# Kernel optimization log

Hardware: AMD Instinct MI355X
Metric: run time of the kernel (lower is better)

The kernel has to match this reference:

```python
import jax, jax.numpy as jnp
import numpy as np

B, N, D, H, CH = 16, 2048, 2, 128, 32
NEG = -1e9


def setup_inputs() -> dict:
    key = jax.random.key(0)
    ks = jax.random.split(key, 24)
    u = lambda k, shape, fan_in: jax.random.uniform(k, shape, jnp.float32,
                                                    -1.0 / np.sqrt(fan_in), 1.0 / np.sqrt(fan_in))
    inp = {
        "features": jax.random.normal(ks[0], (B, N, D), jnp.float32),
        "adj": jax.random.randint(ks[1], (B, N, N), 0, 2, jnp.int32),
        "candidates": jax.random.randint(ks[2], (B, N), 0, 2, jnp.int32).at[:, 0].set(1),
        "action": jnp.zeros((B,), jnp.int32),
        # GCN encoder (3 layers)
        "W1": u(ks[3], (D, H), D), "b1": jnp.zeros((H,), jnp.float32),
        "W2": u(ks[4], (H, H), H), "b2": jnp.zeros((H,), jnp.float32),
        "W3": u(ks[5], (H, H), H), "b3": jnp.zeros((H,), jnp.float32),
        # learned machine state
        "machine_state": jax.random.uniform(ks[6], (H,), jnp.float32, -1.0, 1.0),
        # actor MLP: Linear(3H,H) -> ReLU -> Linear(H,H) -> ReLU -> Linear(H,1)
        "A1": u(ks[7], (3 * H, H), 3 * H), "ab1": u(ks[8], (H,), 3 * H),
        "A2": u(ks[9], (H, H), H), "ab2": u(ks[10], (H,), H),
        "A3": u(ks[11], (H, 1), H), "ab3": u(ks[12], (1,), H),
        # critic MLP: Linear(H,CH) -> ReLU -> Linear(CH,1)
        "C1": u(ks[13], (H, CH), H), "cb1": u(ks[14], (CH,), H),
        "C2": u(ks[15], (CH, 1), CH), "cb2": u(ks[16], (1,), CH),
    }
    return inp


def _gcn_propagation_matrix(adj):
    # Faithful to PyG GCNConv(add_self_loops=True) fed edges from dense_to_sparse
    # with edge attrs discarded (all weights 1).
    A = (adj != 0).astype(jnp.float32)                      # (B,N,N), A[b,j,i]: edge j->i
    A = jnp.maximum(A, jnp.eye(N, dtype=jnp.float32))       # add_remaining_self_loops
    deg = A.sum(axis=1)                                     # (B,N) incoming degree per target i
    dis = jax.lax.rsqrt(deg)                                # deg >= 1 due to self loops
    # S[b,j,i] = dis[j] * A[j,i] * dis[i]
    return dis[:, :, None] * A * dis[:, None, :]


def reference(features, adj, candidates, action,
              W1, b1, W2, b2, W3, b3, machine_state,
              A1, ab1, A2, ab2, A3, ab3, C1, cb1, C2, cb2):
    S = _gcn_propagation_matrix(adj)
    h = features
    for W, b in ((W1, b1), (W2, b2), (W3, b3)):
        # out[b,i,:] = sum_j S[b,j,i] * (h W)[b,j,:]
        h = jax.nn.relu(jnp.einsum('bji,bjd->bid', S, h @ W) + b)
    pool = h.mean(axis=1)                                   # (B,H) global mean pool

    concat = jnp.concatenate(
        [h,
         jnp.broadcast_to(pool[:, None, :], h.shape),
         jnp.broadcast_to(machine_state[None, None, :], h.shape)], axis=-1)  # (B,N,3H)
    a = jax.nn.relu(concat @ A1 + ab1)
    a = jax.nn.relu(a @ A2 + ab2)
    scores = ((a @ A3 + ab3)[..., 0]) * 10.0                # (B,N)

    probs_sm = jax.nn.softmax(scores, axis=1)               # softmax over jobs
    logits = jnp.where(candidates != 0, probs_sm, NEG)      # masked_fill(~candidates, -inf)
    logp = jax.nn.log_softmax(logits, axis=1)               # Categorical(logits=...)
    log_prob = jnp.take_along_axis(logp, action[:, None].astype(jnp.int32), axis=1)[:, 0]
    p = jnp.exp(logp)
    entropy = -(p * logp).sum(axis=1)

    value = jax.nn.relu(pool @ C1 + cb1) @ C2 + cb2         # (B,1)
    return action, log_prob, entropy, value
```

## Files before the change

### kernel.cpp

```cpp
#include <hip/hip_runtime.h>
#include <hip/hip_bf16.h>
#include <stdint.h>

#define B_  16
#define N_  2048
#define D_  2
#define H_  128
#define CH_ 32
#define NEG_ (-1e9f)

typedef __attribute__((ext_vector_type(8))) short bf16x8;
typedef __attribute__((ext_vector_type(4))) float f32x4;
typedef unsigned short u16;

__device__ inline u16 f2bf(float f){
    union { __hip_bfloat16 h; u16 u; } cv;
    cv.h = __float2bfloat16(f);
    return cv.u;
}
__device__ inline float bf2f(u16 v){ return __uint_as_float(((unsigned)v) << 16); }

__device__ inline void gld16(const u16* g, u16* l){
    __builtin_amdgcn_global_load_lds(
        (const __attribute__((address_space(1))) unsigned int*)(const void*)g,
        (__attribute__((address_space(3))) unsigned int*)(void*)l, 16, 0, 0);
}

__global__ __launch_bounds__(256) void k_prep(const int* __restrict__ adj,
                                              u16* __restrict__ ATbf,
                                              float* __restrict__ degF){
    int i0 = blockIdx.x * 64, j0 = blockIdx.y * 64, b = blockIdx.z;
    __shared__ u16 tile[64 * 72];
    __shared__ float degP[256];
    int t = threadIdx.x;
    const int* ap = adj + (size_t)b * N_ * N_;
    #pragma unroll
    for (int it = 0; it < 4; ++it){
        int jj = it * 16 + (t >> 4);
        int gi0 = (t & 15) * 4;
        int4 a4 = *(const int4*)&ap[(size_t)(j0 + jj) * N_ + i0 + gi0];
        int gj = j0 + jj;
        tile[(gi0 + 0) * 72 + jj] = (a4.x != 0 || gj == i0 + gi0 + 0) ? (u16)0x3F80 : (u16)0;
        tile[(gi0 + 1) * 72 + jj] = (a4.y != 0 || gj == i0 + gi0 + 1) ? (u16)0x3F80 : (u16)0;
        tile[(gi0 + 2) * 72 + jj] = (a4.z != 0 || gj == i0 + gi0 + 2) ? (u16)0x3F80 : (u16)0;
        tile[(gi0 + 3) * 72 + jj] = (a4.w != 0 || gj == i0 + gi0 + 3) ? (u16)0x3F80 : (u16)0;
    }
    __syncthreads();
    {
        int ii = t & 63, q = t >> 6;
        float s = 0.f;
        #pragma unroll
        for (int k = 0; k < 16; ++k) s += (tile[ii * 72 + q * 16 + k] ? 1.f : 0.f);
        degP[t] = s;
    }
    __syncthreads();
    if (t < 64){
        float s = degP[t] + degP[t + 64] + degP[t + 128] + degP[t + 192];
        atomicAdd(&degF[b * N_ + i0 + t], s);
    }
    u16* op = ATbf + (size_t)b * N_ * N_;
    #pragma unroll
    for (int it = 0; it < 2; ++it){
        int idx = it * 256 + t;
        int io = idx >> 3, jo = (idx & 7) * 8;
        *(uint4*)&op[(size_t)(i0 + io) * N_ + j0 + jo] = *(const uint4*)&tile[io * 72 + jo];
    }
}

__global__ __launch_bounds__(256) void k_misc(const float* __restrict__ degF,
                                              float* __restrict__ dis,
                                              const float* __restrict__ W2, u16* __restrict__ WT2,
                                              const float* __restrict__ W3, u16* __restrict__ WT3,
                                              const float* __restrict__ A1, u16* __restrict__ A1aT,
                                              const float* __restrict__ A2, u16* __restrict__ A2T){
    int bx = blockIdx.x;
    if (bx < 128){
        int i = bx * 256 + threadIdx.x;
        dis[i] = rsqrtf(degF[i]);
        return;
    }
    int q = (bx - 128) >> 6;
    const float* s; u16* d;
    switch (q){
        case 0: s = W2; d = WT2; break;
        case 1: s = W3; d = WT3; break;
        case 2: s = A1; d = A1aT; break;
        default: s = A2; d = A2T; break;
    }
    int idx = ((bx - 128) & 63) * 256 + threadIdx.x;
    int hp = idx >> 7, k = idx & 127;
    d[hp * 128 + k] = f2bf(s[k * 128 + hp]);
}

__global__ __launch_bounds__(256) void k_y1(const float* __restrict__ feat,
                                            const float* __restrict__ W1,
                                            const float* __restrict__ dis,
                                            u16* __restrict__ YT){
    int j = blockIdx.x * 256 + threadIdx.x;
    int h = blockIdx.y, b = blockIdx.z;
    float f0 = feat[((size_t)b * N_ + j) * D_ + 0];
    float f1 = feat[((size_t)b * N_ + j) * D_ + 1];
    float v = dis[b * N_ + j] * (f0 * W1[h] + f1 * W1[H_ + h]);
    YT[(size_t)b * H_ * N_ + (size_t)h * N_ + j] = f2bf(v);
}

template<int MODE>
__global__ __launch_bounds__(512) void k_layer(const u16* __restrict__ ATbf,
                                               const u16* __restrict__ Yin,
                                               const float* __restrict__ dis,
                                               const float* __restrict__ bias,
                                               const u16* __restrict__ WT,
                                               u16* __restrict__ Yout,
                                               u16* __restrict__ h3,
                                               float* __restrict__ poolF){
    int bid = blockIdx.x;
    int b = bid & 15, i0 = (bid >> 4) * 128;
    const u16* Ab = ATbf + (size_t)b * N_ * N_ + (size_t)i0 * N_;
    const u16* Bb = Yin  + (size_t)b * H_ * N_;
    __shared__ __align__(16) u16 ABs[16384];
    __shared__ __align__(16) u16 Hs[128 * 136];
    u16* As = ABs;
    u16* Bs = ABs + 8192;
    int t = threadIdx.x, w = t >> 6, lane = t & 63, quad = lane >> 4, l16 = lane & 15;
    int srow = lane >> 3, scol = (lane & 7) * 8;
    f32x4 acc[8];
    #pragma unroll
    for (int nt = 0; nt < 8; ++nt) acc[nt] = (f32x4){0.f, 0.f, 0.f, 0.f};

    for (int k0 = 0; k0 < N_; k0 += 64){
        #pragma unroll
        for (int it = 0; it < 4; ++it){
            int chunk = w * 4 + it;
            if (chunk < 16)
                gld16(Ab + (size_t)(chunk * 8 + srow) * N_ + k0 + scol, As + chunk * 512);
            else
                gld16(Bb + (size_t)((chunk - 16) * 8 + srow) * N_ + k0 + scol, Bs + (chunk - 16) * 512);
        }
        __syncthreads();
        #pragma unroll
        for (int kc = 0; kc < 2; ++kc){
            bf16x8 af = *(const bf16x8*)&As[(w * 16 + l16) * 64 + kc * 32 + quad * 8];
            #pragma unroll
            for (int nt = 0; nt < 8; ++nt){
                bf16x8 bv = *(const bf16x8*)&Bs[(nt * 16 + l16) * 64 + kc * 32 + quad * 8];
                acc[nt] = __builtin_amdgcn_mfma_f32_16x16x32_bf16(af, bv, acc[nt], 0, 0, 0);
            }
        }
        __syncthreads();
    }

    if (MODE == 0){
        #pragma unroll
        for (int it = 0; it < 4; ++it){
            int chunk = w * 4 + it;
            gld16(WT + (size_t)(chunk * 4 + (lane >> 4)) * 128 + (lane & 15) * 8,
                  ABs + chunk * 512);
        }
    }
    #pragma unroll
    for (int r = 0; r < 4; ++r){
        int m = w * 16 + quad * 4 + r;
        float dsc = dis[b * N_ + i0 + m];
        #pragma unroll
        for (int nt = 0; nt < 8; ++nt){
            int n = nt * 16 + l16;
            float v = dsc * acc[nt][r] + bias[n];
            Hs[m * 136 + n] = f2bf(v > 0.f ? v : 0.f);
        }
    }
    __syncthreads();

    if (MODE == 0){
        f32x4 a2[8];
        #pragma unroll
        for (int nt = 0; nt < 8; ++nt) a2[nt] = (f32x4){0.f, 0.f, 0.f, 0.f};
        #pragma unroll
        for (int kc = 0; kc < 4; ++kc){
            bf16x8 af = *(const bf16x8*)&Hs[(w * 16 + l16) * 136 + kc * 32 + quad * 8];
            #pragma unroll
            for (int nt = 0; nt < 8; ++nt){
                bf16x8 bv = *(const bf16x8*)&ABs[(nt * 16 + l16) * 128 + kc * 32 + quad * 8];
                a2[nt] = __builtin_amdgcn_mfma_f32_16x16x32_bf16(af, bv, a2[nt], 0, 0, 0);
            }
        }
        __syncthreads();
        #pragma unroll
        for (int r = 0; r < 4; ++r){
            int m = w * 16 + quad * 4 + r;
            float dsc = dis[b * N_ + i0 + m];
            #pragma unroll
            for (int nt = 0; nt < 8; ++nt)
                Hs[m * 136 + nt * 16 + l16] = f2bf(dsc * a2[nt][r]);
        }
        __syncthreads();
        size_t obase = (size_t)b * H_ * N_ + i0;
        int j = t & 127, hq = t >> 7;
        #pragma unroll 8
        for (int rep = 0; rep < 32; ++rep){
            int hrow = hq + rep * 4;
            Yout[obase + (size_t)hrow * N_ + j] = Hs[j * 136 + hrow];
        }
    } else {
        #pragma unroll
        for (int rep = 0; rep < 4; ++rep){
            int idx = rep * 512 + t;
            int row = idx >> 3, col = (idx & 7) * 8;
            *(uint4*)&h3[((size_t)b * N_ + i0 + row) * H_ + col] = *(const uint4*)&Hs[row * 136 + col];
        }
        __shared__ float pred[512];
        int n = t & 127, rq = t >> 7;
        float ps = 0.f;
        #pragma unroll 8
        for (int r = 0; r < 32; ++r) ps += bf2f(Hs[(rq * 32 + r) * 136 + n]);
        pred[t] = ps;
        __syncthreads();
        if (t < 128)
            atomicAdd(&poolF[b * H_ + t],
                      (pred[t] + pred[t + 128] + pred[t + 256] + pred[t + 384]) * (1.f / N_));
    }
}

__global__ __launch_bounds__(256) void k_cv(const float* __restrict__ poolF,
                                            const float* __restrict__ ms,
                                            const float* __restrict__ A1,
                                            const float* __restrict__ ab1,
                                            const float* __restrict__ C1,
                                            const float* __restrict__ cb1,
                                            const float* __restrict__ C2,
                                            const float* __restrict__ cb2,
                                            float* __restrict__ cvec,
                                            float* __restrict__ out){
    int b = blockIdx.x, t = threadIdx.x;
    __shared__ float pl[128], msl[128], v1[32];
    if (t < 128){ pl[t] = poolF[b * H_ + t]; msl[t] = ms[t]; }
    __syncthreads();
    if (t < 128){
        float c = ab1[t];
        for (int k = 0; k < 128; ++k)
            c += pl[k] * A1[(128 + k) * H_ + t] + msl[k] * A1[(256 + k) * H_ + t];
        cvec[b * H_ + t] = c;
    } else if (t < 160){
        int cc = t - 128;
        float v = cb1[cc];
        for (int k = 0; k < 128; ++k) v += pl[k] * C1[k * CH_ + cc];
        v1[cc] = v > 0.f ? v : 0.f;
    }
    __syncthreads();
    if (t == 0){
        float v = cb2[0];
        for (int c = 0; c < CH_; ++c) v += v1[c] * C2[c];
        out[48 + b] = v;
    }
}

__global__ __launch_bounds__(256) void k_actor(const u16* __restrict__ h3,
                                               const u16* __restrict__ A1aT,
                                               const u16* __restrict__ A2T,
                                               const float* __restrict__ cvec,
                                               const float* __restrict__ ab2,
                                               const float* __restrict__ A3,
                                               const float* __restrict__ ab3,
                                               float* __restrict__ scores){
    int b = blockIdx.x, i0 = blockIdx.y * 128;
    const u16* Ab = h3 + ((size_t)b * N_ + i0) * H_;
    __shared__ __align__(16) u16 As[128 * 72];
    __shared__ __align__(16) u16 Bs[128 * 72];
    __shared__ __align__(16) u16 M1[128 * 136];
    __shared__ float sLDS[128];
    int t = threadIdx.x, w = t >> 6, lane = t & 63, quad = lane >> 4, l16 = lane & 15;
    int sr = t >> 3, sc = (t & 7) * 8;
    f32x4 acc[2][8];
    #pragma unroll
    for (int mt = 0; mt < 2; ++mt)
        #pragma unroll
        for (int nt = 0; nt < 8; ++nt) acc[mt][nt] = (f32x4){0.f, 0.f, 0.f, 0.f};
    for (int k0 = 0; k0 < H_; k0 += 64){
        #pragma unroll
        for (int it = 0; it < 4; ++it){
            int r = sr + it * 32;
            *(uint4*)&As[r * 72 + sc] = *(const uint4*)&Ab[(size_t)r * H_ + k0 + sc];
            *(uint4*)&Bs[r * 72 + sc] = *(const uint4*)&A1aT[(size_t)r * H_ + k0 + sc];
        }
        __syncthreads();
        #pragma unroll
        for (int kc = 0; kc < 2; ++kc){
            bf16x8 af[2];
            #pragma unroll
            for (int mt = 0; mt < 2; ++mt)
                af[mt] = *(const bf16x8*)&As[(w * 32 + mt * 16 + l16) * 72 + kc * 32 + quad * 8];
            #pragma unroll
            for (int nt = 0; nt < 8; ++nt){
                bf16x8 bfr = *(const bf16x8*)&Bs[(nt * 16 + l16) * 72 + kc * 32 + quad * 8];
                #pragma unroll
                for (int mt = 0; mt < 2; ++mt)
                    acc[mt][nt] = __builtin_amdgcn_mfma_f32_16x16x32_bf16(af[mt], bfr, acc[mt][nt], 0, 0, 0);
            }
        }
        __syncthreads();
    }
    const float* cv = cvec + b * H_;
    #pragma unroll
    for (int mt = 0; mt < 2; ++mt)
        #pragma unroll
        for (int r = 0; r < 4; ++r){
            int m = w * 32 + mt * 16 + quad * 4 + r;
            #pragma unroll
            for (int nt = 0; nt < 8; ++nt){
                int n = nt * 16 + l16;
                float v = acc[mt][nt][r] + cv[n];
                M1[m * 136 + n] = f2bf(v > 0.f ? v : 0.f);
                acc[mt][nt][r] = 0.f;
            }
        }
    if (t < 128) sLDS[t] = 0.f;
    for (int k0 = 0; k0 < H_; k0 += 64){
        #pragma unroll
        for (int it = 0; it < 4; ++it){
            int r = sr + it * 32;
            *(uint4*)&Bs[r * 72 + sc] = *(const uint4*)&A2T[(size_t)r * H_ + k0 + sc];
        }
        __syncthreads();
        #pragma unroll
        for (int kc = 0; kc < 2; ++kc){
            bf16x8 af[2];
            #pragma unroll
            for (int mt = 0; mt < 2; ++mt)
                af[mt] = *(const bf16x8*)&M1[(w * 32 + mt * 16 + l16) * 136 + k0 + kc * 32 + quad * 8];
            #pragma unroll
            for (int nt = 0; nt < 8; ++nt){
                bf16x8 bfr = *(const bf16x8*)&Bs[(nt * 16 + l16) * 72 + kc * 32 + quad * 8];
                #pragma unroll
                for (int mt = 0; mt < 2; ++mt)
                    acc[mt][nt] = __builtin_amdgcn_mfma_f32_16x16x32_bf16(af[mt], bfr, acc[mt][nt], 0, 0, 0);
            }
        }
        __syncthreads();
    }
    #pragma unroll
    for (int mt = 0; mt < 2; ++mt)
        #pragma unroll
        for (int r = 0; r < 4; ++r){
            int m = w * 32 + mt * 16 + quad * 4 + r;
            float part = 0.f;
            #pragma unroll
            for (int nt = 0; nt < 8; ++nt){
                int n = nt * 16 + l16;
                float v = acc[mt][nt][r] + ab2[n];
                v = v > 0.f ? v : 0.f;
                part += v * A3[n];
            }
            atomicAdd(&sLDS[m], part);
        }
    __syncthreads();
    if (t < 128) scores[(size_t)b * N_ + i0 + t] = (sLDS[t] + ab3[0]) * 10.f;
}

__device__ inline float wredS(float v){
    #pragma unroll
    for (int o = 32; o; o >>= 1) v += __shfl_xor(v, o, 64);
    return v;
}
__device__ inline float wredM(float v){
    #pragma unroll
    for (int o = 32; o; o >>= 1) v = fmaxf(v, __shfl_xor(v, o, 64));
    return v;
}

__global__ __launch_bounds__(256) void k_sm(const float* __restrict__ scores,
                                            const int* __restrict__ cand,
                                            const int* __restrict__ action,
                                            float* __restrict__ out){
    int b = blockIdx.x, t = threadIdx.x;
    __shared__ float sc[N_];
    __shared__ float red[4];
    __shared__ float lps;
    const float* sp = scores + (size_t)b * N_;
    const int*   cp = cand   + (size_t)b * N_;
    float mx = -1e30f;
    for (int i = t; i < N_; i += 256){ float v = sp[i]; sc[i] = v; mx = fmaxf(mx, v); }
    mx = wredM(mx);
    if ((t & 63) == 0) red[t >> 6] = mx;
    __syncthreads();
    mx = fmaxf(fmaxf(red[0], red[1]), fmaxf(red[2], red[3]));
    __syncthreads();
    float se = 0.f;
    for (int i = t; i < N_; i += 256) se += expf(sc[i] - mx);
    se = wredS(se);
    if ((t & 63) == 0) red[t >> 6] = se;
    __syncthreads();
    float s1 = red[0] + red[1] + red[2] + red[3];
    __syncthreads();
    float inv = 1.f / s1;
    float m2 = -1e30f;
    for (int i = t; i < N_; i += 256){
        float p = expf(sc[i] - mx) * inv;
        sc[i] = p;
        if (cp[i] != 0) m2 = fmaxf(m2, p);
    }
    m2 = wredM(m2);
    if ((t & 63) == 0) red[t >> 6] = m2;
    __syncthreads();
    m2 = fmaxf(fmaxf(red[0], red[1]), fmaxf(red[2], red[3]));
    __syncthreads();
    float s2 = 0.f;
    for (int i = t; i < N_; i += 256) if (cp[i] != 0) s2 += expf(sc[i] - m2);
    s2 = wredS(s2);
    if ((t & 63) == 0) red[t >> 6] = s2;
    __syncthreads();
    float lse = m2 + logf(red[0] + red[1] + red[2] + red[3]);
    __syncthreads();
    int a = action[b];
    float ent = 0.f;
    for (int i = t; i < N_; i += 256){
        float lp = (cp[i] != 0 ? sc[i] : NEG_) - lse;
        float pe = expf(lp);
        ent -= pe * lp;
        if (i == a) lps = lp;
    }
    ent = wredS(ent);
    if ((t & 63) == 0) red[t >> 6] = ent;
    __syncthreads();
    if (t == 0){
        out[b]      = (float)a;
        out[16 + b] = lps;
        out[32 + b] = red[0] + red[1] + red[2] + red[3];
    }
}

extern "C" void kernel_launch(void* const* d_in, const int* in_sizes, int n_in,
                              void* d_out, int out_size, void* d_ws, size_t ws_size,
                              hipStream_t stream) {
    const float* feat = (const float*)d_in[0];
    const int*   adj  = (const int*)d_in[1];
    const int*   cand = (const int*)d_in[2];
    const int*   act  = (const int*)d_in[3];
    const float* W1   = (const float*)d_in[4];
    const float* b1   = (const float*)d_in[5];
    const float* W2   = (const float*)d_in[6];
    const float* b2   = (const float*)d_in[7];
    const float* W3   = (const float*)d_in[8];
    const float* b3   = (const float*)d_in[9];
    const float* ms   = (const float*)d_in[10];
    const float* A1   = (const float*)d_in[11];
    const float* ab1  = (const float*)d_in[12];
    const float* A2   = (const float*)d_in[13];
    const float* ab2  = (const float*)d_in[14];
    const float* A3   = (const float*)d_in[15];
    const float* ab3  = (const float*)d_in[16];
    const float* C1   = (const float*)d_in[17];
    const float* cb1  = (const float*)d_in[18];
    const float* C2   = (const float*)d_in[19];
    const float* cb2  = (const float*)d_in[20];
    float* out = (float*)d_out;

    char* w8 = (char*)d_ws;
    size_t off = 0;
    auto alloc = [&](size_t bytes){ void* p = w8 + off; off += (bytes + 255) & ~(size_t)255; return p; };
    u16*   ATbf  = (u16*)  alloc((size_t)B_ * N_ * N_ * 2);
    u16*   YTa   = (u16*)  alloc((size_t)B_ * H_ * N_ * 2);
    u16*   YTb   = (u16*)  alloc((size_t)B_ * H_ * N_ * 2);
    u16*   hbuf  = (u16*)  alloc((size_t)B_ * N_ * H_ * 2);
    float* degF  = (float*)alloc((size_t)B_ * N_ * 4);
    float* poolF = (float*)alloc((size_t)B_ * H_ * 4);
    float* dis   = (float*)alloc((size_t)B_ * N_ * 4);
    float* cvec  = (float*)alloc((size_t)B_ * H_ * 4);
    float* scr   = (float*)alloc((size_t)B_ * N_ * 4);
    u16*   WT2   = (u16*)  alloc((size_t)H_ * H_ * 2);
    u16*   WT3   = (u16*)  alloc((size_t)H_ * H_ * 2);
    u16*   A1aT  = (u16*)  alloc((size_t)H_ * H_ * 2);
    u16*   A2T   = (u16*)  alloc((size_t)H_ * H_ * 2);

    hipMemsetAsync(degF, 0, (size_t)B_ * N_ * 4 + (size_t)B_ * H_ * 4, stream);

    k_prep<<<dim3(32, 32, 16), 256, 0, stream>>>(adj, ATbf, degF);
    k_misc<<<dim3(384), 256, 0, stream>>>(degF, dis, W2, WT2, W3, WT3, A1, A1aT, A2, A2T);
    k_y1  <<<dim3(8, 128, 16), 256, 0, stream>>>(feat, W1, dis, YTa);

    k_layer<0><<<dim3(256), 512, 0, stream>>>(ATbf, YTa, dis, b1, WT2, YTb, nullptr, nullptr);
    k_layer<0><<<dim3(256), 512, 0, stream>>>(ATbf, YTb, dis, b2, WT3, YTa, nullptr, nullptr);
    k_layer<1><<<dim3(256), 512, 0, stream>>>(ATbf, YTa, dis, b3, nullptr, nullptr, hbuf, poolF);

    k_cv  <<<dim3(16), 256, 0, stream>>>(poolF, ms, A1, ab1, C1, cb1, C2, cb2, cvec, out);
    k_actor<<<dim3(16, 16), 256, 0, stream>>>(hbuf, A1aT, A2T, cvec, ab2, A3, ab3, scr);
    k_sm  <<<dim3(16), 256, 0, stream>>>(scr, cand, act, out);
}
```

Before: 656.5 us.

## Retile GCN layer kernel to 64-row blocks with 2x4 warp tiles and swizzled LDS

The propagation GEMM kernel moves from 128-row tiles with 512 threads to 64-row tiles with 256 threads and 512 blocks. Each wave now computes a 32x64 sub-tile, so A fragments are reused across the N tiles. An XOR swizzle is added to the LDS layout to avoid bank conflicts, and the weight matrix is preloaded into a padded separate LDS buffer. Doubling the grid improves CU coverage (512 blocks on 256 CUs), at the cost of re-reading the Y operand twice as often.

```diff
diff --git a/kernel.cpp b/kernel.cpp
--- a/kernel.cpp
+++ b/kernel.cpp
@@ -105,109 +105,133 @@
 }
 
 template<int MODE>
-__global__ __launch_bounds__(512) void k_layer(const u16* __restrict__ ATbf,
-                                               const u16* __restrict__ Yin,
-                                               const float* __restrict__ dis,
-                                               const float* __restrict__ bias,
-                                               const u16* __restrict__ WT,
-                                               u16* __restrict__ Yout,
-                                               u16* __restrict__ h3,
-                                               float* __restrict__ poolF){
+__global__ __launch_bounds__(256, 2) void k_layer(const u16* __restrict__ ATbf,
+                                                  const u16* __restrict__ Yin,
+                                                  const float* __restrict__ dis,
+                                                  const float* __restrict__ bias,
+                                                  const u16* __restrict__ WT,
+                                                  u16* __restrict__ Yout,
+                                                  u16* __restrict__ h3,
+                                                  float* __restrict__ poolF){
     int bid = blockIdx.x;
-    int b = bid & 15, i0 = (bid >> 4) * 128;
+    int b = bid & 15, i0 = (bid >> 4) * 64;
     const u16* Ab = ATbf + (size_t)b * N_ * N_ + (size_t)i0 * N_;
     const u16* Bb = Yin  + (size_t)b * H_ * N_;
-    __shared__ __align__(16) u16 ABs[16384];
-    __shared__ __align__(16) u16 Hs[128 * 136];
-    u16* As = ABs;
-    u16* Bs = ABs + 8192;
+    __shared__ __align__(16) u16 As[64 * 64];
+    __shared__ __align__(16) u16 Bs[128 * 64];
+    __shared__ __align__(16) u16 Hs[64 * 136];
+    __shared__ __align__(16) u16 Ws[MODE == 0 ? 128 * 136 : 16];
     int t = threadIdx.x, w = t >> 6, lane = t & 63, quad = lane >> 4, l16 = lane & 15;
-    int srow = lane >> 3, scol = (lane & 7) * 8;
-    f32x4 acc[8];
-    #pragma unroll
-    for (int nt = 0; nt < 8; ++nt) acc[nt] = (f32x4){0.f, 0.f, 0.f, 0.f};
+    int mr = w & 1, nc = w >> 1;
+    int srow = lane >> 3;
+    int xcol = ((lane & 7) ^ srow) * 8;
+    int x7 = l16 & 7;
+
+    if (MODE == 0){
+        #pragma unroll
+        for (int it = 0; it < 8; ++it){
+            int e = it * 256 + t;
+            int row = e >> 4, c8 = e & 15;
+            *(uint4*)&Ws[row * 136 + c8 * 8] = *(const uint4*)&WT[row * 128 + c8 * 8];
+        }
+    }
+
+    f32x4 acc[2][4];
+    #pragma unroll
+    for (int mt = 0; mt < 2; ++mt)
+        #pragma unroll
+        for (int nt = 0; nt < 4; ++nt) acc[mt][nt] = (f32x4){0.f, 0.f, 0.f, 0.f};
 
     for (int k0 = 0; k0 < N_; k0 += 64){
         #pragma unroll
-        for (int it = 0; it < 4; ++it){
-            int chunk = w * 4 + it;
-            if (chunk < 16)
-                gld16(Ab + (size_t)(chunk * 8 + srow) * N_ + k0 + scol, As + chunk * 512);
+        for (int it = 0; it < 6; ++it){
+            int chunk = w * 6 + it;
+            if (chunk < 8)
+                gld16(Ab + (size_t)(chunk * 8 + srow) * N_ + k0 + xcol, As + chunk * 512);
             else
-                gld16(Bb + (size_t)((chunk - 16) * 8 + srow) * N_ + k0 + scol, Bs + (chunk - 16) * 512);
+                gld16(Bb + (size_t)((chunk - 8) * 8 + srow) * N_ + k0 + xcol, Bs + (chunk - 8) * 512);
         }
         __syncthreads();
         #pragma unroll
         for (int kc = 0; kc < 2; ++kc){
-            bf16x8 af = *(const bf16x8*)&As[(w * 16 + l16) * 64 + kc * 32 + quad * 8];
-            #pragma unroll
-            for (int nt = 0; nt < 8; ++nt){
-                bf16x8 bv = *(const bf16x8*)&Bs[(nt * 16 + l16) * 64 + kc * 32 + quad * 8];
-                acc[nt] = __builtin_amdgcn_mfma_f32_16x16x32_bf16(af, bv, acc[nt], 0, 0, 0);
-            }
-        }
-        __syncthreads();
-    }
+            int gx = ((kc * 4 + quad) ^ x7) * 8;
+            bf16x8 af[2];
+            #pragma unroll
+            for (int mt = 0; mt < 2; ++mt)
+                af[mt] = *(const bf16x8*)&As[(mr * 32 + mt * 16 + l16) * 64 + gx];
+            #pragma unroll
+            for (int nt = 0; nt < 4; ++nt){
+                bf16x8 bv = *(const bf16x8*)&Bs[(nc * 64 + nt * 16 + l16) * 64 + gx];
+                #pragma unroll
+                for (int mt = 0; mt < 2; ++mt)
+                    acc[mt][nt] = __builtin_amdgcn_mfma_f32_16x16x32_bf16(af[mt], bv, acc[mt][nt], 0, 0, 0);
+            }
+        }
+        __syncthreads();
+    }
+
+    #pragma unroll
+    for (int mt = 0; mt < 2; ++mt)
+        #pragma unroll
+        for (int r = 0; r < 4; ++r){
+            int m = mr * 32 + mt * 16 + quad * 4 + r;
+            float dsc = dis[b * N_ + i0 + m];
+            #pragma unroll
+            for (int nt = 0; nt < 4; ++nt){
+                int n = nc * 64 + nt * 16 + l16;
+                float v = dsc * acc[mt][nt][r] + bias[n];
+                Hs[m * 136 + n] = f2bf(v > 0.f ? v : 0.f);
+            }
+        }
+    __syncthreads();
 
     if (MODE == 0){
-        #pragma unroll
-        for (int it = 0; it < 4; ++it){
-            int chunk = w * 4 + it;
-            gld16(WT + (size_t)(chunk * 4 + (lane >> 4)) * 128 + (lane & 15) * 8,
-                  ABs + chunk * 512);
-        }
-    }
-    #pragma unroll
-    for (int r = 0; r < 4; ++r){
-        int m = w * 16 + quad * 4 + r;
-        float dsc = dis[b * N_ + i0 + m];
-        #pragma unroll
-        for (int nt = 0; nt < 8; ++nt){
-            int n = nt * 16 + l16;
-            float v = dsc * acc[nt][r] + bias[n];
-            Hs[m * 136 + n] = f2bf(v > 0.f ? v : 0.f);
-        }
-    }
-    __syncthreads();
-
-    if (MODE == 0){
-        f32x4 a2[8];
-        #pragma unroll
-        for (int nt = 0; nt < 8; ++nt) a2[nt] = (f32x4){0.f, 0.f, 0.f, 0.f};
+        f32x4 a2[2][4];
+        #pragma unroll
+        for (int mt = 0; mt < 2; ++mt)
+            #pragma unroll
+            for (int nt = 0; nt < 4; ++nt) a2[mt][nt] = (f32x4){0.f, 0.f, 0.f, 0.f};
         #pragma unroll
         for (int kc = 0; kc < 4; ++kc){
-            bf16x8 af = *(const bf16x8*)&Hs[(w * 16 + l16) * 136 + kc * 32 + quad * 8];
-            #pragma unroll
-            for (int nt = 0; nt < 8; ++nt){
-                bf16x8 bv = *(const bf16x8*)&ABs[(nt * 16 + l16) * 128 + kc * 32 + quad * 8];
-                a2[nt] = __builtin_amdgcn_mfma_f32_16x16x32_bf16(af, bv, a2[nt], 0, 0, 0);
-            }
-        }
-        __syncthreads();
-        #pragma unroll
-        for (int r = 0; r < 4; ++r){
-            int m = w * 16 + quad * 4 + r;
-            float dsc = dis[b * N_ + i0 + m];
-            #pragma unroll
-            for (int nt = 0; nt < 8; ++nt)
-                Hs[m * 136 + nt * 16 + l16] = f2bf(dsc * a2[nt][r]);
-        }
+            bf16x8 af[2];
+            #pragma unroll
+            for (int mt = 0; mt < 2; ++mt)
+                af[mt] = *(const bf16x8*)&Hs[(mr * 32 + mt * 16 + l16) * 136 + kc * 32 + quad * 8];
+            #pragma unroll
+            for (int nt = 0; nt < 4; ++nt){
+                bf16x8 bv = *(const bf16x8*)&Ws[(nc * 64 + nt * 16 + l16) * 136 + kc * 32 + quad * 8];
+                #pragma unroll
+                for (int mt = 0; mt < 2; ++mt)
+                    a2[mt][nt] = __builtin_amdgcn_mfma_f32_16x16x32_bf16(af[mt], bv, a2[mt][nt], 0, 0, 0);
+            }
+        }
+        __syncthreads();
+        #pragma unroll
+        for (int mt = 0; mt < 2; ++mt)
+            #pragma unroll
+            for (int r = 0; r < 4; ++r){
+                int m = mr * 32 + mt * 16 + quad * 4 + r;
+                float dsc = dis[b * N_ + i0 + m];
+                #pragma unroll
+                for (int nt = 0; nt < 4; ++nt)
+                    Hs[m * 136 + nc * 64 + nt * 16 + l16] = f2bf(dsc * a2[mt][nt][r]);
+            }
         __syncthreads();
         size_t obase = (size_t)b * H_ * N_ + i0;
-        int j = t & 127, hq = t >> 7;
+        int j = t & 63, hq = t >> 6;
         #pragma unroll 8
         for (int rep = 0; rep < 32; ++rep){
-            int hrow = hq + rep * 4;
+            int hrow = hq * 32 + rep;
             Yout[obase + (size_t)hrow * N_ + j] = Hs[j * 136 + hrow];
         }
     } else {
         #pragma unroll
         for (int rep = 0; rep < 4; ++rep){
-            int idx = rep * 512 + t;
-            int row = idx >> 3, col = (idx & 7) * 8;
-            *(uint4*)&h3[((size_t)b * N_ + i0 + row) * H_ + col] = *(const uint4*)&Hs[row * 136 + col];
-        }
-        __shared__ float pred[512];
+            int e = rep * 256 + t;
+            int row = e >> 4, c8 = e & 15;
+            *(uint4*)&h3[((size_t)b * N_ + i0 + row) * H_ + c8 * 8] = *(const uint4*)&Hs[row * 136 + c8 * 8];
+        }
+        __shared__ float pred[256];
         int n = t & 127, rq = t >> 7;
         float ps = 0.f;
         #pragma unroll 8
@@ -215,8 +239,7 @@
         pred[t] = ps;
         __syncthreads();
         if (t < 128)
-            atomicAdd(&poolF[b * H_ + t],
-                      (pred[t] + pred[t + 128] + pred[t + 256] + pred[t + 384]) * (1.f / N_));
+            atomicAdd(&poolF[b * H_ + t], (pred[t] + pred[t + 128]) * (1.f / N_));
     }
 }
 
@@ -476,9 +499,9 @@
     k_misc<<<dim3(384), 256, 0, stream>>>(degF, dis, W2, WT2, W3, WT3, A1, A1aT, A2, A2T);
     k_y1  <<<dim3(8, 128, 16), 256, 0, stream>>>(feat, W1, dis, YTa);
 
-    k_layer<0><<<dim3(256), 512, 0, stream>>>(ATbf, YTa, dis, b1, WT2, YTb, nullptr, nullptr);
-    k_layer<0><<<dim3(256), 512, 0, stream>>>(ATbf, YTb, dis, b2, WT3, YTa, nullptr, nullptr);
-    k_layer<1><<<dim3(256), 512, 0, stream>>>(ATbf, YTa, dis, b3, nullptr, nullptr, hbuf, poolF);
+    k_layer<0><<<dim3(512), 256, 0, stream>>>(ATbf, YTa, dis, b1, WT2, YTb, nullptr, nullptr);
+    k_layer<0><<<dim3(512), 256, 0, stream>>>(ATbf, YTb, dis, b2, WT3, YTa, nullptr, nullptr);
+    k_layer<1><<<dim3(512), 256, 0, stream>>>(ATbf, YTa, dis, b3, nullptr, nullptr, hbuf, poolF);
 
     k_cv  <<<dim3(16), 256, 0, stream>>>(poolF, ms, A1, ab1, C1, cb1, C2, cb2, cvec, out);
     k_actor<<<dim3(16, 16), 256, 0, stream>>>(hbuf, A1aT, A2T, cvec, ab2, A3, ab3, scr);
```

After: 582.7 us. 1.13x faster.
